# Performance work log

Hardware: AMD Instinct MI355X
Metric: run time of the kernel (lower is better)

Reference implementation:

```python
import jax, jax.numpy as jnp
import numpy as np
import math

BS, SEQ = 2048, 50
REL, ETYPE = 6, 4
ATT, HEADS, HEAD = 64, 4, 16
HID, OUT = 128, 64


def setup_inputs() -> dict:
    key = jax.random.key(0)
    ks = jax.random.split(key, 20)
    d = {}
    d['input_seqs'] = jax.random.normal(ks[0], (BS, SEQ, 3, 3, REL), jnp.float32)
    d['input_edge_types'] = jax.random.uniform(ks[1], (BS, SEQ, 3, 3, ETYPE), jnp.float32)
    d['input_masks'] = jax.random.randint(ks[2], (BS, SEQ, 3, 3), 0, 2, jnp.int32)
    def lin(k, fin, fout):
        k1, k2 = jax.random.split(k)
        bound = 1.0 / math.sqrt(fin)
        W = jax.random.uniform(k1, (fout, fin), jnp.float32, -bound, bound)
        b = jax.random.uniform(k2, (fout,), jnp.float32, -bound, bound)
        return W, b
    d['W_fus'], d['b_fus'] = lin(ks[3], REL + ETYPE + 9, 64)
    d['Wk'], d['bk'] = lin(ks[4], REL, ATT)
    d['Wq'], d['bq'] = lin(ks[5], 64, ATT)
    d['Wv'], d['bv'] = lin(ks[6], 64, ATT)
    bound = 1.0 / math.sqrt(HID)
    d['W_ih'] = jax.random.uniform(ks[7], (4 * HID, ATT), jnp.float32, -bound, bound)
    d['W_hh'] = jax.random.uniform(ks[8], (4 * HID, HID), jnp.float32, -bound, bound)
    d['b_ih'] = jax.random.uniform(ks[9], (4 * HID,), jnp.float32, -bound, bound)
    d['b_hh'] = jax.random.uniform(ks[10], (4 * HID,), jnp.float32, -bound, bound)
    d['W_out'], d['b_out'] = lin(ks[11], HID, OUT)
    return d


def _lstm_last(xs, W_ih, W_hh, b_ih, b_hh):
    # xs: (seq, bs, ATT); torch LSTM gate order i,f,g,o. Returns last hidden state.
    b = b_ih + b_hh
    def step(carry, x):
        h, c = carry
        gates = x @ W_ih.T + h @ W_hh.T + b
        i, f, g, o = jnp.split(gates, 4, axis=-1)
        i, f, o = jax.nn.sigmoid(i), jax.nn.sigmoid(f), jax.nn.sigmoid(o)
        g = jnp.tanh(g)
        c = f * c + i * g
        h = o * jnp.tanh(c)
        return (h, c), None
    h0 = jnp.zeros((xs.shape[1], HID), xs.dtype)
    (h, _), _ = jax.lax.scan(step, (h0, h0), xs)
    return h


def reference(input_seqs, input_edge_types, input_masks, W_fus, b_fus, Wk, bk, Wq, bq, Wv, bv, W_ih, W_hh, b_ih, b_hh, W_out, b_out):
    bs, seq = input_seqs.shape[0], input_seqs.shape[1]
    # location one-hot for the 3x3 neighborhood
    loc = jnp.broadcast_to(jnp.eye(9, dtype=input_seqs.dtype).reshape(3, 3, 9), (bs, seq, 3, 3, 9))
    edge_info = jnp.concatenate([input_seqs, input_edge_types, loc], axis=-1)
    edge_info = edge_info @ W_fus.T + b_fus                 # (bs, seq, 3, 3, 64)
    edge_info = edge_info.reshape(bs, seq, 9, 64)
    self_info = input_seqs[:, :, 1, 1]                       # (bs, seq, REL)
    # key from self state (same for all 9 slots), query/value from edge info
    key = (self_info @ Wk.T + bk).reshape(bs, seq, 1, HEADS, HEAD)     # broadcast over 9
    query = (edge_info @ Wq.T + bq).reshape(bs, seq, 9, HEADS, HEAD)
    value = (edge_info @ Wv.T + bv).reshape(bs, seq, 9, HEADS, HEAD)
    # att: dot over head dim -> (bs, seq, heads, 9)
    att = jnp.einsum('bsnhd,bsnhd->bshn', jnp.broadcast_to(key, query.shape), query) / math.sqrt(HEAD)
    mask9 = input_masks.reshape(bs, seq, 1, 9)               # broadcast over heads
    att = jnp.where(mask9 == 0, jnp.float32(-1e10), att)
    att = jax.nn.softmax(att, axis=-1)                       # (bs, seq, heads, 9)
    ctx = jnp.einsum('bshn,bsnhd->bshd', att, value)         # (bs, seq, heads, head)
    ctx = ctx.reshape(bs, seq, ATT).transpose(1, 0, 2)       # (seq, bs, ATT)
    h_last = _lstm_last(ctx, W_ih, W_hh, b_ih, b_hh)         # (bs, HID)
    return h_last @ W_out.T + b_out                          # (bs, OUT)
```

## Files before the change

### kernel.cpp

```cpp
#include <hip/hip_runtime.h>
#include <math.h>

#define BS   2048
#define SEQ  50
#define NPOS (BS * SEQ)

typedef __attribute__((ext_vector_type(8))) short bf16x8;
typedef __attribute__((ext_vector_type(4))) float f32x4;

__device__ __forceinline__ float sigf(float x) { return 1.0f / (1.0f + __expf(-x)); }
__device__ __forceinline__ float tanhfast(float x) {
    float e = __expf(2.0f * x);
    return 1.0f - 2.0f / (e + 1.0f);
}
__device__ __forceinline__ unsigned short bfrn(float x) {
    unsigned int u = __float_as_uint(x);
    u += 0x7FFFu + ((u >> 16) & 1u);
    return (unsigned short)(u >> 16);
}
__device__ __forceinline__ float bf2f(unsigned short h) {
    return __uint_as_float(((unsigned int)h) << 16);
}

#define FMA4(A, X, W) \
    A = fmaf((X).x, (W).x, A); A = fmaf((X).y, (W).y, A); \
    A = fmaf((X).z, (W).z, A); A = fmaf((X).w, (W).w, A);

__device__ float G_d[640];
__device__ float D_d[576];
__device__ float Wvf_d[640];
__device__ float Ce_d[576];

__global__ __launch_bounds__(512) void prep_all(
    const float* __restrict__ Wih, const float* __restrict__ Whh,
    bf16x8* __restrict__ whF, bf16x8* __restrict__ wiF,
    const float* __restrict__ Wf, const float* __restrict__ bf,
    const float* __restrict__ Wq, const float* __restrict__ bq,
    const float* __restrict__ Wv)
{
    int id = blockIdx.x * 512 + threadIdx.x;
    if (id < 24576) {
        const float* src;
        bf16x8* dst;
        int p;
        if (id < 16384) {
            int l = id & 63, frag = id >> 6;
            p = frag & 1;
            int kc = (frag >> 1) & 3, ti = (frag >> 3) & 3, w = frag >> 5;
            int n  = (w + 8 * ti) * 16 + (l & 15);
            int k0 = kc * 32 + (l >> 4) * 8;
            src = &Whh[n * 128 + k0];
            dst = &whF[frag * 64 + l];
        } else {
            int id2 = id - 16384;
            int l = id2 & 63, frag = id2 >> 6;
            p = frag & 1;
            int kc = (frag >> 1) & 1, tile = frag >> 2;
            int n  = tile * 16 + (l & 15);
            int k0 = kc * 32 + (l >> 4) * 8;
            src = &Wih[n * 64 + k0];
            dst = &wiF[frag * 64 + l];
        }
        bf16x8 v;
        #pragma unroll
        for (int j = 0; j < 8; ++j) {
            float x = src[j];
            unsigned short hi = bfrn(x);
            unsigned short r  = p ? bfrn(x - bf2f(hi)) : hi;
            v[j] = (short)r;
        }
        *dst = v;
        return;
    }
    int i = id - 24576;
    if (i >= 2432) return;
    if (i < 640) {
        int n = i / 10, k = i % 10;
        float s = 0.f;
        #pragma unroll 8
        for (int j = 0; j < 64; ++j) s = fmaf(Wq[n * 64 + j], Wf[j * 19 + k], s);
        G_d[i] = s;
    } else if (i < 1216) {
        int i2 = i - 640;
        int e = i2 >> 6, n = i2 & 63;
        float s = bq[n];
        #pragma unroll 8
        for (int j = 0; j < 64; ++j)
            s = fmaf(Wf[j * 19 + 10 + e] + bf[j], Wq[n * 64 + j], s);
        D_d[i2] = s;
    } else if (i < 1856) {
        int i3 = i - 1216;
        int o = i3 / 10, k = i3 % 10;
        float s = 0.f;
        #pragma unroll 8
        for (int j = 0; j < 64; ++j) s = fmaf(Wv[o * 64 + j], Wf[j * 19 + k], s);
        Wvf_d[i3] = s;
    } else {
        int i4 = i - 1856;
        int o = i4 / 9, e = i4 % 9;
        float s = 0.f;
        #pragma unroll 8
        for (int j = 0; j < 64; ++j)
            s = fmaf(Wf[j * 19 + 10 + e] + bf[j], Wv[o * 64 + j], s);
        Ce_d[i4] = s;
    }
}

__global__ __launch_bounds__(64, 4) void edge_attn_ctx(
    const float* __restrict__ seqs,
    const float* __restrict__ ets,
    const int*   __restrict__ masks,
    const float* __restrict__ Wk, const float* __restrict__ bk,
    const float* __restrict__ bv,
    float* __restrict__ ctx)
{
    const int o   = threadIdx.x;
    const int h_o = o >> 4;
    const int lg  = (o < 40) ? o : 0;
    const int gh  = lg / 10, gk = lg % 10;
    const int la  = (o < 36) ? o : 0;
    const int ah  = la / 9,  ae = la % 9;

    const float* wkp = &Wk[o * 6];
    const float wk0 = wkp[0], wk1 = wkp[1], wk2 = wkp[2],
                wk3 = wkp[3], wk4 = wkp[4], wk5 = wkp[5];
    const float bkr = bk[o];

    float Greg[16], Dreg[16];
    #pragma unroll
    for (int d = 0; d < 16; ++d) Greg[d] = G_d[(gh * 16 + d) * 10 + gk];
    #pragma unroll
    for (int d = 0; d < 16; ++d) Dreg[d] = D_d[ae * 64 + ah * 16 + d];
    float Wvfr[10];
    #pragma unroll
    for (int k = 0; k < 10; ++k) Wvfr[k] = Wvf_d[o * 10 + k];
    const float bvr = bv[o];
    float Cer[9];
    #pragma unroll
    for (int e = 0; e < 9; ++e) Cer[e] = Ce_d[o * 9 + e] + bvr;

    __shared__ float s_seq[54], s_et[36], s_key[64], s_g[40];
    __shared__ float s_att[36], s_exp[36], s_rbar[40];
    __shared__ int   s_mask[9];

    float r_seq = 0.f, r_et = 0.f; int r_mask = 0;
    {
        int p0 = blockIdx.x;
        if (o < 54) r_seq  = seqs[p0 * 54 + o];
        if (o < 36) r_et   = ets[p0 * 36 + o];
        if (o < 9)  r_mask = masks[p0 * 9 + o];
    }

    for (int p = blockIdx.x; p < NPOS; p += gridDim.x) {
        if (o < 54) s_seq[o]  = r_seq;
        if (o < 36) s_et[o]   = r_et;
        if (o < 9)  s_mask[o] = r_mask;
        __syncthreads();

        {
            int pn = p + gridDim.x;
            if (pn < NPOS) {
                if (o < 54) r_seq  = seqs[pn * 54 + o];
                if (o < 36) r_et   = ets[pn * 36 + o];
                if (o < 9)  r_mask = masks[pn * 9 + o];
            }
        }
        float key = bkr;
        key = fmaf(s_seq[24], wk0, key);
        key = fmaf(s_seq[25], wk1, key);
        key = fmaf(s_seq[26], wk2, key);
        key = fmaf(s_seq[27], wk3, key);
        key = fmaf(s_seq[28], wk4, key);
        key = fmaf(s_seq[29], wk5, key);
        s_key[o] = key;
        __syncthreads();

        float tt = 0.f;
        if (o < 40) {
            float g = 0.f;
            #pragma unroll
            for (int d = 0; d < 16; ++d) g = fmaf(Greg[d], s_key[gh * 16 + d], g);
            s_g[o] = g;
        }
        if (o < 36) {
            #pragma unroll
            for (int d = 0; d < 16; ++d) tt = fmaf(Dreg[d], s_key[ah * 16 + d], tt);
        }
        __syncthreads();

        float a = 0.f;
        if (o < 36) {
            a = tt;
            #pragma unroll
            for (int k = 0; k < 6; ++k) a = fmaf(s_seq[ae * 6 + k], s_g[ah * 10 + k], a);
            #pragma unroll
            for (int k = 0; k < 4; ++k) a = fmaf(s_et[ae * 4 + k], s_g[ah * 10 + 6 + k], a);
            a *= 0.25f;
            if (s_mask[ae] == 0) a = -1.0e10f;
            s_att[o] = a;
        }
        __syncthreads();

        float ex = 0.f;
        if (o < 36) {
            float mx = s_att[ah * 9 + 0];
            #pragma unroll
            for (int e = 1; e < 9; ++e) mx = fmaxf(mx, s_att[ah * 9 + e]);
            ex = __expf(a - mx);
            s_exp[o] = ex;
        }
        __syncthreads();

        if (o < 40) {
            float rb = 0.f;
            #pragma unroll
            for (int e = 0; e < 9; ++e) {
                float x = (gk < 6) ? s_seq[e * 6 + gk] : s_et[e * 4 + (gk - 6)];
                rb = fmaf(s_exp[gh * 9 + e], x, rb);
            }
            s_rbar[o] = rb;
        }
        __syncthreads();

        {
            float ssum = 0.f;
            #pragma unroll
            for (int e = 0; e < 9; ++e) ssum += s_exp[h_o * 9 + e];
            float acc = 0.f;
            #pragma unroll
            for (int k = 0; k < 10; ++k) acc = fmaf(s_rbar[h_o * 10 + k], Wvfr[k], acc);
            #pragma unroll
            for (int e = 0; e < 9; ++e) acc = fmaf(s_exp[h_o * 9 + e], Cer[e], acc);
            ctx[p * 64 + o] = acc * (1.0f / ssum);
        }
    }
}

#define MFMA16(A, B, C) __builtin_amdgcn_mfma_f32_16x16x32_bf16(A, B, C, 0, 0, 0)
#define MM4(F, W0, W1, W2, W3) \
    a0 = MFMA16(F, W0, a0); a1 = MFMA16(F, W1, a1); \
    a2 = MFMA16(F, W2, a2); a3 = MFMA16(F, W3, a3);

#define HPASS \
    MM4(hfh[0], whr[0][0][0], whr[1][0][0], whr[2][0][0], whr[3][0][0]) \
    MM4(hfh[1], whr[0][1][0], whr[1][1][0], whr[2][1][0], whr[3][1][0]) \
    MM4(hfh[2], whr[0][2][0], whr[1][2][0], whr[2][2][0], whr[3][2][0]) \
    MM4(hfh[3], whr[0][3][0], whr[1][3][0], whr[2][3][0], whr[3][3][0]) \
    MM4(hfl[0], whr[0][0][0], whr[1][0][0], whr[2][0][0], whr[3][0][0]) \
    MM4(hfl[1], whr[0][1][0], whr[1][1][0], whr[2][1][0], whr[3][1][0]) \
    MM4(hfl[2], whr[0][2][0], whr[1][2][0], whr[2][2][0], whr[3][2][0]) \
    MM4(hfl[3], whr[0][3][0], whr[1][3][0], whr[2][3][0], whr[3][3][0]) \
    MM4(hfh[0], whr[0][0][1], whr[1][0][1], whr[2][0][1], whr[3][0][1]) \
    MM4(hfh[1], whr[0][1][1], whr[1][1][1], whr[2][1][1], whr[3][1][1]) \
    MM4(hfh[2], whr[0][2][1], whr[1][2][1], whr[2][2][1], whr[3][2][1]) \
    MM4(hfh[3], whr[0][3][1], whr[1][3][1], whr[2][3][1], whr[3][3][1])

#define REDIST_E(ch, g0, g1) { \
    float s2_ = __shfl_xor(ch[2], 32), s3_ = __shfl_xor(ch[3], 32); \
    g0 = lolq ? ch[0] : s2_;  g1 = lolq ? ch[1] : s3_; }
#define REDIST_O(ch, g0, g1) { \
    float s0_ = __shfl_xor(ch[0], 32), s1_ = __shfl_xor(ch[1], 32); \
    g0 = lolq ? s0_ : ch[2];  g1 = lolq ? s1_ : ch[3]; }

#define PWBODY(gi0,gf0,gg0,go0,gi1,gf1,gg1,go1, WB0, WB1) { \
    float i0_ = sigf(gi0 + bi), f0_ = sigf(gf0 + bff); \
    float gA_ = tanhfast(gg0 + bg), o0_ = sigf(go0 + bo); \
    c20 = fmaf(f0_, c20, i0_ * gA_); \
    float hv0_ = o0_ * tanhfast(c20); \
    float i1_ = sigf(gi1 + bi), f1_ = sigf(gf1 + bff); \
    float gB_ = tanhfast(gg1 + bg), o1_ = sigf(go1 + bo); \
    c21 = fmaf(f1_, c21, i1_ * gB_); \
    float hv1_ = o1_ * tanhfast(c21); \
    unsigned short hh0_ = bfrn(hv0_), hh1_ = bfrn(hv1_); \
    unsigned short hl0_ = bfrn(hv0_ - bf2f(hh0_)), hl1_ = bfrn(hv1_ - bf2f(hh1_)); \
    *(unsigned short*)((char*)s_hh + (WB0)) = hh0_; \
    *(unsigned short*)((char*)s_hl + (WB0)) = hl0_; \
    *(unsigned short*)((char*)s_hh + (WB1)) = hh1_; \
    *(unsigned short*)((char*)s_hl + (WB1)) = hl1_; }

__global__ __launch_bounds__(512, 2) void lstm_mfma(
    const float*  __restrict__ ctx,
    const bf16x8* __restrict__ whF,
    const bf16x8* __restrict__ wiFg,
    const float*  __restrict__ b_ih, const float* __restrict__ b_hh,
    const float*  __restrict__ W_out, const float* __restrict__ b_out,
    float* __restrict__ out)
{
    const int t  = threadIdx.x;
    const int w  = t >> 6, l = t & 63;
    const int lm = l & 15, lq = l >> 4;
    const int row0 = blockIdx.x * 8;

    __shared__ bf16x8 s_wi[8192];
    __shared__ unsigned short s_xh[1024], s_xl[1024];
    __shared__ unsigned short s_hh[4096], s_hl[4096];

    for (int i = t; i < 8192; i += 512) s_wi[i] = wiFg[i];
    for (int i = t; i < 1024; i += 512) { s_xh[i] = 0; s_xl[i] = 0; }
    for (int i = t; i < 4096; i += 512) { s_hh[i] = 0; s_hl[i] = 0; }

    bf16x8 whr[4][4][2];
    #pragma unroll
    for (int ti = 0; ti < 4; ++ti)
        #pragma unroll
        for (int kc = 0; kc < 4; ++kc)
            #pragma unroll
            for (int p = 0; p < 2; ++p)
                whr[ti][kc][p] = whF[(((w * 4 + ti) * 4 + kc) * 2 + p) * 64 + l];

    const int m = w * 16 + lm;
    const float bi  = b_ih[m]       + b_hh[m];
    const float bff = b_ih[128 + m] + b_hh[128 + m];
    const float bg  = b_ih[256 + m] + b_hh[256 + m];
    const float bo  = b_ih[384 + m] + b_hh[384 + m];

    const int  urb  = ((lq & 1) << 2) | (lq & 2);
    const bool lolq = (lq < 2);
    float c20 = 0.f, c21 = 0.f;

    const int xrow  = t >> 5;
    const int xl32  = t & 31;
    const int srow  = xrow & 7;
    const int spair = xrow >> 3;
    const float2* ctx2 = (const float2*)ctx;
    const int xbase = (row0 + srow) * SEQ + spair;
    const int xwb   = xrow * 128 + ((4 * xl32) ^ ((xrow & 7) << 4));
    const int swzr  = (lm & 7) << 4;
    const int hwb_m = 32 * w + 2 * lm;
    const int wb0e = 4096 + (8 + urb) * 256 + (hwb_m ^ (urb << 4));
    const int wb1e = 4096 + (9 + urb) * 256 + (hwb_m ^ ((urb + 1) << 4));
    const int wb0o = urb * 256 + (hwb_m ^ (urb << 4));
    const int wb1o = (urb + 1) * 256 + (hwb_m ^ ((urb + 1) << 4));

    float2 xv = ctx2[xbase * 32 + xl32];

    for (int u = 0; u < SEQ / 2; ++u) {
        {
            unsigned short xh0 = bfrn(xv.x), xh1 = bfrn(xv.y);
            unsigned short xl0 = bfrn(xv.x - bf2f(xh0)), xl1 = bfrn(xv.y - bf2f(xh1));
            *(unsigned int*)((char*)s_xh + xwb) = (unsigned int)xh0 | ((unsigned int)xh1 << 16);
            *(unsigned int*)((char*)s_xl + xwb) = (unsigned int)xl0 | ((unsigned int)xl1 << 16);
        }
        __syncthreads();

        float2 xvn = make_float2(0.f, 0.f);
        if (u + 1 < SEQ / 2) xvn = ctx2[(xbase + 2 * u + 2) * 32 + xl32];

        bf16x8 hfh[4], hfl[4];
        if (u > 0) {
            #pragma unroll
            for (int kc = 0; kc < 4; ++kc) {
                int b = lm * 256 + ((kc * 64 + lq * 16) ^ swzr);
                hfh[kc] = *(const bf16x8*)((const char*)s_hh + b);
                hfl[kc] = *(const bf16x8*)((const char*)s_hl + b);
            }
        }
        bf16x8 xfh[2], xfl[2];
        #pragma unroll
        for (int kc = 0; kc < 2; ++kc) {
            int b = lm * 128 + ((kc * 64 + lq * 16) ^ swzr);
            xfh[kc] = *(const bf16x8*)((const char*)s_xh + b);
            xfl[kc] = *(const bf16x8*)((const char*)s_xl + b);
        }

        f32x4 a0 = {0.f,0.f,0.f,0.f}, a1 = a0, a2 = a0, a3 = a0;

        if (u > 0) { HPASS }

        #pragma unroll
        for (int kc = 0; kc < 2; ++kc) {
            bf16x8 wihi[4], wilo[4];
            #pragma unroll
            for (int ti = 0; ti < 4; ++ti) {
                int base = (((w + 8 * ti) * 2 + kc) * 2) * 64 + l;
                wihi[ti] = s_wi[base];
                wilo[ti] = s_wi[base + 64];
            }
            MM4(xfh[kc], wihi[0], wihi[1], wihi[2], wihi[3])
            MM4(xfl[kc], wihi[0], wihi[1], wihi[2], wihi[3])
            MM4(xfh[kc], wilo[0], wilo[1], wilo[2], wilo[3])
        }

        {
            float gi0, gi1, gf0, gf1, gg0, gg1, go0, go1;
            REDIST_E(a0, gi0, gi1)
            REDIST_E(a1, gf0, gf1)
            REDIST_E(a2, gg0, gg1)
            REDIST_E(a3, go0, go1)
            PWBODY(gi0, gf0, gg0, go0, gi1, gf1, gg1, go1, wb0e, wb1e)
        }

        __syncthreads();
        #pragma unroll
        for (int kc = 0; kc < 4; ++kc) {
            int b = 4096 + lm * 256 + ((kc * 64 + lq * 16) ^ swzr);
            hfh[kc] = *(const bf16x8*)((const char*)s_hh + b);
            hfl[kc] = *(const bf16x8*)((const char*)s_hl + b);
        }
        HPASS

        {
            float gi0, gi1, gf0, gf1, gg0, gg1, go0, go1;
            REDIST_O(a0, gi0, gi1)
            REDIST_O(a1, gf0, gf1)
            REDIST_O(a2, gg0, gg1)
            REDIST_O(a3, go0, go1)
            PWBODY(gi0, gf0, gg0, go0, gi1, gf1, gg1, go1, wb0o, wb1o)
        }
        xv = xvn;
    }
    __syncthreads();

    {
        const int row = t >> 5;
        if (row < 8) {
            const int j0 = t & 31, j1 = (t & 31) + 32;
            const int rswz = (row & 7) << 4;
            float accA = b_out[j0], accB = b_out[j1];
            #pragma unroll
            for (int kq = 0; kq < 16; ++kq) {
                int b = row * 256 + ((kq * 16) ^ rswz);
                bf16x8 hh8 = *(const bf16x8*)((const char*)s_hh + b);
                bf16x8 hl8 = *(const bf16x8*)((const char*)s_hl + b);
                #pragma unroll
                for (int e = 0; e < 8; ++e) {
                    float h = bf2f((unsigned short)hh8[e]) + bf2f((unsigned short)hl8[e]);
                    int k = kq * 8 + e;
                    accA = fmaf(h, W_out[j0 * 128 + k], accA);
                    accB = fmaf(h, W_out[j1 * 128 + k], accB);
                }
            }
            out[(row0 + row) * 64 + j0] = accA;
            out[(row0 + row) * 64 + j1] = accB;
        }
    }
}

extern "C" void kernel_launch(void* const* d_in, const int* in_sizes, int n_in,
                              void* d_out, int out_size, void* d_ws, size_t ws_size,
                              hipStream_t stream) {
    (void)in_sizes; (void)n_in; (void)out_size; (void)ws_size;
    const float* seqs  = (const float*)d_in[0];
    const float* ets   = (const float*)d_in[1];
    const int*   masks = (const int*)d_in[2];
    const float* Wf  = (const float*)d_in[3];
    const float* bf  = (const float*)d_in[4];
    const float* Wk  = (const float*)d_in[5];
    const float* bk  = (const float*)d_in[6];
    const float* Wq  = (const float*)d_in[7];
    const float* bq  = (const float*)d_in[8];
    const float* Wv  = (const float*)d_in[9];
    const float* bv  = (const float*)d_in[10];
    const float* Wih = (const float*)d_in[11];
    const float* Whh = (const float*)d_in[12];
    const float* bih = (const float*)d_in[13];
    const float* bhh = (const float*)d_in[14];
    const float* Wo  = (const float*)d_in[15];
    const float* bo  = (const float*)d_in[16];

    char* ws = (char*)d_ws;
    bf16x8* whF = (bf16x8*)(ws);
    bf16x8* wiF = (bf16x8*)(ws + 262144);
    float*  ctx = (float*) (ws + 262144 + 131072);

    hipLaunchKernelGGL(prep_all, dim3(53), dim3(512), 0, stream,
                       Wih, Whh, whF, wiF, Wf, bf, Wq, bq, Wv);
    hipLaunchKernelGGL(edge_attn_ctx, dim3(4096), dim3(64), 0, stream,
                       seqs, ets, masks, Wk, bk, bv, ctx);
    hipLaunchKernelGGL(lstm_mfma, dim3(256), dim3(512), 0, stream,
                       ctx, whF, wiF, bih, bhh, Wo, bo, (float*)d_out);
}
```

Before: 246.2 us.

## Fold key projection into precomputed attention tables and run one position per wave

Precomputes combined tables Ag and Bd that absorb Wk/bk into the query-side weight products, so each position computes attention logits straight from the 6 self features instead of first building a 64-wide key and two 16-term dot products. The edge kernel now runs two independent waves per 128-thread block, each handling its own position stream with per-wave shared buffers. Block-wide __syncthreads calls are replaced by wave barriers. This cuts per-position ALU work and synchronisation cost, but the prep kernel gains redundant inner loops and the lockstep-within-a-wave assumption must hold for correctness.

Result: slower. 286.0 us (+16.2%).

```diff
diff --git a/kernel.cpp b/kernel.cpp
--- a/kernel.cpp
+++ b/kernel.cpp
@@ -26,17 +26,18 @@
     A = fmaf((X).x, (W).x, A); A = fmaf((X).y, (W).y, A); \
     A = fmaf((X).z, (W).z, A); A = fmaf((X).w, (W).w, A);
 
-__device__ float G_d[640];
-__device__ float D_d[576];
 __device__ float Wvf_d[640];
 __device__ float Ce_d[576];
+__device__ float Ag_d[280];
+__device__ float Bd_d[252];
 
 __global__ __launch_bounds__(512) void prep_all(
     const float* __restrict__ Wih, const float* __restrict__ Whh,
     bf16x8* __restrict__ whF, bf16x8* __restrict__ wiF,
     const float* __restrict__ Wf, const float* __restrict__ bf,
     const float* __restrict__ Wq, const float* __restrict__ bq,
-    const float* __restrict__ Wv)
+    const float* __restrict__ Wv,
+    const float* __restrict__ Wk, const float* __restrict__ bk)
 {
     int id = blockIdx.x * 512 + threadIdx.x;
     if (id < 24576) {
@@ -73,64 +74,72 @@
         return;
     }
     int i = id - 24576;
-    if (i >= 2432) return;
+    if (i >= 1748) return;
     if (i < 640) {
-        int n = i / 10, k = i % 10;
-        float s = 0.f;
-        #pragma unroll 8
-        for (int j = 0; j < 64; ++j) s = fmaf(Wq[n * 64 + j], Wf[j * 19 + k], s);
-        G_d[i] = s;
-    } else if (i < 1216) {
-        int i2 = i - 640;
-        int e = i2 >> 6, n = i2 & 63;
-        float s = bq[n];
-        #pragma unroll 8
-        for (int j = 0; j < 64; ++j)
-            s = fmaf(Wf[j * 19 + 10 + e] + bf[j], Wq[n * 64 + j], s);
-        D_d[i2] = s;
-    } else if (i < 1856) {
-        int i3 = i - 1216;
-        int o = i3 / 10, k = i3 % 10;
+        int o = i / 10, k = i % 10;
         float s = 0.f;
         #pragma unroll 8
         for (int j = 0; j < 64; ++j) s = fmaf(Wv[o * 64 + j], Wf[j * 19 + k], s);
-        Wvf_d[i3] = s;
-    } else {
-        int i4 = i - 1856;
-        int o = i4 / 9, e = i4 % 9;
+        Wvf_d[i] = s;
+    } else if (i < 1216) {
+        int i2 = i - 640;
+        int o = i2 / 9, e = i2 % 9;
         float s = 0.f;
         #pragma unroll 8
         for (int j = 0; j < 64; ++j)
             s = fmaf(Wf[j * 19 + 10 + e] + bf[j], Wv[o * 64 + j], s);
-        Ce_d[i4] = s;
+        Ce_d[i2] = s;
+    } else if (i < 1496) {
+        int i3 = i - 1216;
+        int h = i3 / 70, rem = i3 % 70, k = rem / 7, j = rem % 7;
+        float s = 0.f;
+        for (int d = 0; d < 16; ++d) {
+            int n = h * 16 + d;
+            float Gnk = 0.f;
+            #pragma unroll 8
+            for (int mm = 0; mm < 64; ++mm)
+                Gnk = fmaf(Wq[n * 64 + mm], Wf[mm * 19 + k], Gnk);
+            float wkj = (j < 6) ? Wk[n * 6 + j] : bk[n];
+            s = fmaf(wkj, Gnk, s);
+        }
+        Ag_d[i3] = s;
+    } else {
+        int i4 = i - 1496;
+        int e = i4 / 28, rem = i4 % 28, h = rem / 7, j = rem % 7;
+        float s = 0.f;
+        for (int d = 0; d < 16; ++d) {
+            int n = h * 16 + d;
+            float Den = bq[n];
+            #pragma unroll 8
+            for (int mm = 0; mm < 64; ++mm)
+                Den = fmaf(Wf[mm * 19 + 10 + e] + bf[mm], Wq[n * 64 + mm], Den);
+            float wkj = (j < 6) ? Wk[n * 6 + j] : bk[n];
+            s = fmaf(wkj, Den, s);
+        }
+        Bd_d[i4] = s;
     }
 }
 
-__global__ __launch_bounds__(64, 4) void edge_attn_ctx(
+__global__ __launch_bounds__(128, 6) void edge_attn_ctx(
     const float* __restrict__ seqs,
     const float* __restrict__ ets,
     const int*   __restrict__ masks,
-    const float* __restrict__ Wk, const float* __restrict__ bk,
     const float* __restrict__ bv,
     float* __restrict__ ctx)
 {
-    const int o   = threadIdx.x;
+    const int wid = threadIdx.x >> 6;
+    const int o   = threadIdx.x & 63;
     const int h_o = o >> 4;
     const int lg  = (o < 40) ? o : 0;
     const int gh  = lg / 10, gk = lg % 10;
     const int la  = (o < 36) ? o : 0;
     const int ah  = la / 9,  ae = la % 9;
 
-    const float* wkp = &Wk[o * 6];
-    const float wk0 = wkp[0], wk1 = wkp[1], wk2 = wkp[2],
-                wk3 = wkp[3], wk4 = wkp[4], wk5 = wkp[5];
-    const float bkr = bk[o];
-
-    float Greg[16], Dreg[16];
+    float Agr[7], Bdr[7];
     #pragma unroll
-    for (int d = 0; d < 16; ++d) Greg[d] = G_d[(gh * 16 + d) * 10 + gk];
+    for (int j = 0; j < 7; ++j) Agr[j] = Ag_d[(gh * 10 + gk) * 7 + j];
     #pragma unroll
-    for (int d = 0; d < 16; ++d) Dreg[d] = D_d[ae * 64 + ah * 16 + d];
+    for (int j = 0; j < 7; ++j) Bdr[j] = Bd_d[(ae * 4 + ah) * 7 + j];
     float Wvfr[10];
     #pragma unroll
     for (int k = 0; k < 10; ++k) Wvfr[k] = Wvf_d[o * 10 + k];
@@ -139,100 +148,99 @@
     #pragma unroll
     for (int e = 0; e < 9; ++e) Cer[e] = Ce_d[o * 9 + e] + bvr;
 
-    __shared__ float s_seq[54], s_et[36], s_key[64], s_g[40];
-    __shared__ float s_att[36], s_exp[36], s_rbar[40];
-    __shared__ int   s_mask[9];
+    __shared__ float s_seq[2][54], s_et[2][36], s_g[2][40];
+    __shared__ float s_att[2][36], s_exp[2][36], s_rbar[2][40];
+    __shared__ int   s_mask[2][9];
+    float* sq = s_seq[wid];  float* se = s_et[wid];  float* sg = s_g[wid];
+    float* sa = s_att[wid];  float* sx = s_exp[wid]; float* sr = s_rbar[wid];
+    int*   sm = s_mask[wid];
+
+    const int stream = blockIdx.x * 2 + wid;
 
     float r_seq = 0.f, r_et = 0.f; int r_mask = 0;
-    {
-        int p0 = blockIdx.x;
-        if (o < 54) r_seq  = seqs[p0 * 54 + o];
-        if (o < 36) r_et   = ets[p0 * 36 + o];
-        if (o < 9)  r_mask = masks[p0 * 9 + o];
-    }
-
-    for (int p = blockIdx.x; p < NPOS; p += gridDim.x) {
-        if (o < 54) s_seq[o]  = r_seq;
-        if (o < 36) s_et[o]   = r_et;
-        if (o < 9)  s_mask[o] = r_mask;
-        __syncthreads();
+    if (o < 54) r_seq  = seqs[stream * 54 + o];
+    if (o < 36) r_et   = ets[stream * 36 + o];
+    if (o < 9)  r_mask = masks[stream * 9 + o];
+
+    for (int p = stream; p < NPOS; p += 8192) {
+        if (o < 54) sq[o] = r_seq;
+        if (o < 36) se[o] = r_et;
+        if (o < 9)  sm[o] = r_mask;
+        __builtin_amdgcn_wave_barrier();
 
         {
-            int pn = p + gridDim.x;
+            int pn = p + 8192;
             if (pn < NPOS) {
                 if (o < 54) r_seq  = seqs[pn * 54 + o];
                 if (o < 36) r_et   = ets[pn * 36 + o];
                 if (o < 9)  r_mask = masks[pn * 9 + o];
             }
         }
-        float key = bkr;
-        key = fmaf(s_seq[24], wk0, key);
-        key = fmaf(s_seq[25], wk1, key);
-        key = fmaf(s_seq[26], wk2, key);
-        key = fmaf(s_seq[27], wk3, key);
-        key = fmaf(s_seq[28], wk4, key);
-        key = fmaf(s_seq[29], wk5, key);
-        s_key[o] = key;
-        __syncthreads();
-
+
+        float c0 = sq[24], c1 = sq[25], c2 = sq[26],
+              c3 = sq[27], c4 = sq[28], c5 = sq[29];
         float tt = 0.f;
         if (o < 40) {
-            float g = 0.f;
-            #pragma unroll
-            for (int d = 0; d < 16; ++d) g = fmaf(Greg[d], s_key[gh * 16 + d], g);
-            s_g[o] = g;
+            float g = Agr[6];
+            g = fmaf(c0, Agr[0], g); g = fmaf(c1, Agr[1], g);
+            g = fmaf(c2, Agr[2], g); g = fmaf(c3, Agr[3], g);
+            g = fmaf(c4, Agr[4], g); g = fmaf(c5, Agr[5], g);
+            sg[o] = g;
         }
         if (o < 36) {
-            #pragma unroll
-            for (int d = 0; d < 16; ++d) tt = fmaf(Dreg[d], s_key[ah * 16 + d], tt);
-        }
-        __syncthreads();
+            tt = Bdr[6];
+            tt = fmaf(c0, Bdr[0], tt); tt = fmaf(c1, Bdr[1], tt);
+            tt = fmaf(c2, Bdr[2], tt); tt = fmaf(c3, Bdr[3], tt);
+            tt = fmaf(c4, Bdr[4], tt); tt = fmaf(c5, Bdr[5], tt);
+        }
+        __builtin_amdgcn_wave_barrier();
 
         float a = 0.f;
         if (o < 36) {
             a = tt;
             #pragma unroll
-            for (int k = 0; k < 6; ++k) a = fmaf(s_seq[ae * 6 + k], s_g[ah * 10 + k], a);
-            #pragma unroll
-            for (int k = 0; k < 4; ++k) a = fmaf(s_et[ae * 4 + k], s_g[ah * 10 + 6 + k], a);
+            for (int k = 0; k < 6; ++k) a = fmaf(sq[ae * 6 + k], sg[ah * 10 + k], a);
+            #pragma unroll
+            for (int k = 0; k < 4; ++k) a = fmaf(se[ae * 4 + k], sg[ah * 10 + 6 + k], a);
             a *= 0.25f;
-            if (s_mask[ae] == 0) a = -1.0e10f;
-            s_att[o] = a;
-        }
-        __syncthreads();
+            if (sm[ae] == 0) a = -1.0e10f;
+            sa[o] = a;
+        }
+        __builtin_amdgcn_wave_barrier();
 
         float ex = 0.f;
         if (o < 36) {
-            float mx = s_att[ah * 9 + 0];
-            #pragma unroll
-            for (int e = 1; e < 9; ++e) mx = fmaxf(mx, s_att[ah * 9 + e]);
+            float mx = sa[ah * 9 + 0];
+            #pragma unroll
+            for (int e = 1; e < 9; ++e) mx = fmaxf(mx, sa[ah * 9 + e]);
             ex = __expf(a - mx);
-            s_exp[o] = ex;
-        }
-        __syncthreads();
+            sx[o] = ex;
+        }
+        __builtin_amdgcn_wave_barrier();
 
         if (o < 40) {
             float rb = 0.f;
             #pragma unroll
             for (int e = 0; e < 9; ++e) {
-                float x = (gk < 6) ? s_seq[e * 6 + gk] : s_et[e * 4 + (gk - 6)];
-                rb = fmaf(s_exp[gh * 9 + e], x, rb);
+                float x = (gk < 6) ? sq[e * 6 + gk] : se[e * 4 + (gk - 6)];
+                rb = fmaf(sx[gh * 9 + e], x, rb);
             }
-            s_rbar[o] = rb;
-        }
-        __syncthreads();
+            sr[o] = rb;
+        }
+        __builtin_amdgcn_wave_barrier();
 
         {
             float ssum = 0.f;
             #pragma unroll
-            for (int e = 0; e < 9; ++e) ssum += s_exp[h_o * 9 + e];
+            for (int e = 0; e < 9; ++e) ssum += sx[h_o * 9 + e];
             float acc = 0.f;
             #pragma unroll
-            for (int k = 0; k < 10; ++k) acc = fmaf(s_rbar[h_o * 10 + k], Wvfr[k], acc);
-            #pragma unroll
-            for (int e = 0; e < 9; ++e) acc = fmaf(s_exp[h_o * 9 + e], Cer[e], acc);
+            for (int k = 0; k < 10; ++k) acc = fmaf(sr[h_o * 10 + k], Wvfr[k], acc);
+            #pragma unroll
+            for (int e = 0; e < 9; ++e) acc = fmaf(sx[h_o * 9 + e], Cer[e], acc);
             ctx[p * 64 + o] = acc * (1.0f / ssum);
         }
+        __builtin_amdgcn_wave_barrier();
     }
 }
 
@@ -463,10 +471,10 @@
     bf16x8* wiF = (bf16x8*)(ws + 262144);
     float*  ctx = (float*) (ws + 262144 + 131072);
 
-    hipLaunchKernelGGL(prep_all, dim3(53), dim3(512), 0, stream,
-                       Wih, Whh, whF, wiF, Wf, bf, Wq, bq, Wv);
-    hipLaunchKernelGGL(edge_attn_ctx, dim3(4096), dim3(64), 0, stream,
-                       seqs, ets, masks, Wk, bk, bv, ctx);
+    hipLaunchKernelGGL(prep_all, dim3(52), dim3(512), 0, stream,
+                       Wih, Whh, whF, wiF, Wf, bf, Wq, bq, Wv, Wk, bk);
+    hipLaunchKernelGGL(edge_attn_ctx, dim3(4096), dim3(128), 0, stream,
+                       seqs, ets, masks, bv, ctx);
     hipLaunchKernelGGL(lstm_mfma, dim3(256), dim3(512), 0, stream,
                        ctx, whF, wiF, bih, bhh, Wo, bo, (float*)d_out);
 }
```
